# Kernel tuning notes

Measured on AMD Instinct MI355X. Metric: run time of the kernel, lower is better.

## Reference

```python
import jax, jax.numpy as jnp
import numpy as np

B, G, F = 256, 2048, 128   # batch, graph_size, feat_size (== gcn_dim == k)
RNN_DIM = 512
K = F  # self.k = args.gcn_dim


def setup_inputs() -> dict:
    key = jax.random.key(0)
    k1, k2, k3 = jax.random.split(key, 3)
    node_embs = jax.random.normal(k1, (B, G, F), dtype=jnp.float32)
    mask = jnp.zeros((B, G), dtype=jnp.float32)
    h_t = jax.random.normal(k2, (B, RNN_DIM), dtype=jnp.float32)
    W_map = jax.random.normal(k3, (RNN_DIM, F), dtype=jnp.float32) * (1.0 / np.sqrt(RNN_DIM))
    b_map = jnp.zeros((F,), dtype=jnp.float32)
    return {"node_embs": node_embs, "mask": mask, "h_t": h_t, "W_map": W_map, "b_map": b_map}


def reference(node_embs, mask, h_t, W_map, b_map):
    # mapper: Linear + Tanh -> scorer [B, F]
    scorer = jnp.tanh(h_t @ W_map + b_map)
    # scores = bmm(node_embs, scorer) / ||scorer||  -> [B, G]
    norm = jnp.linalg.norm(scorer, axis=1, keepdims=True)  # [B, 1]
    scores = jnp.einsum('bgf,bf->bg', node_embs, scorer) / norm
    scores = scores + mask
    # top-k over graph dim (mask is all-zero so no -inf filtering/padding needed)
    vals, topk_indices = jax.lax.top_k(scores, K)  # [B, K]
    # gather node embeddings at topk indices, scale by tanh of gathered scores
    gathered = jnp.take_along_axis(node_embs, topk_indices[:, :, None], axis=1)  # [B, K, F]
    out = gathered * jnp.tanh(vals)[:, :, None]  # tanh(scores.gather) == tanh(vals)
    # log-softmax over graph dim, gather at topk, mean -> policy score [B]
    log_probs = jax.nn.log_softmax(scores, axis=-1)
    score = jnp.take_along_axis(log_probs, topk_indices, axis=-1)  # [B, K]
    policy_score = score.mean(axis=1)
    return (jnp.transpose(out, (0, 2, 1)), policy_score)  # ([B, F, K], [B])
```

## Files before the change

kernel.cpp:

```cpp
#include <hip/hip_runtime.h>
#include <cmath>

#define B_ 256
#define G_ 2048
#define F_ 128
#define RNN_ 512
#define K_ 128

__global__ __launch_bounds__(1024) void k_fused(const float* __restrict__ node,
                                                const float* __restrict__ mask,
                                                const float* __restrict__ h_t,
                                                const float* __restrict__ W,
                                                const float* __restrict__ b_map,
                                                float* __restrict__ out,
                                                float* __restrict__ policy) {
    __shared__ __align__(16) float sc[G_];
    __shared__ unsigned hist[2][8][256];
    __shared__ __align__(16) float tile[K_][33];
    __shared__ __align__(16) float sn[F_];
    __shared__ unsigned long long win[K_];
    __shared__ float valk[K_];
    __shared__ float tanhv[K_];
    __shared__ int idxk[K_];
    __shared__ float red16[16];
    __shared__ unsigned long long prefix_sh;
    __shared__ int need_sh;
    __shared__ int done_sh;
    __shared__ int cnt;

    const int b = blockIdx.x;
    const int tid = threadIdx.x;
    const int wv = tid >> 6;
    const int lane = tid & 63;

    float* hsm = &tile[0][0];
    float(*wp)[F_] = (float(*)[F_])(hsm + RNN_);
    if (tid < RNN_) hsm[tid] = h_t[b * RNN_ + tid];
    if (tid == 0) { cnt = 0; done_sh = 0; }
    for (int i = tid; i < 8 * 256; i += 1024) ((unsigned*)hist[0])[i] = 0u;
    __syncthreads();
    {
        const int f = tid & 127;
        const int qu = tid >> 7;
        float acc = 0.f;
        const int r0 = qu * (RNN_ / 8);
#pragma unroll 8
        for (int r = r0; r < r0 + RNN_ / 8; ++r) acc += hsm[r] * W[r * F_ + f];
        wp[qu][f] = acc;
    }
    __syncthreads();
    float tval = 0.f;
    if (tid < F_) {
        float a = b_map[tid];
#pragma unroll
        for (int q = 0; q < 8; ++q) a += wp[q][tid];
        tval = tanhf(a);
    }
    float v = tval * tval;
#pragma unroll
    for (int off = 32; off; off >>= 1) v += __shfl_xor(v, off);
    if (tid == 0) red16[0] = v;
    if (tid == 64) red16[1] = v;
    __syncthreads();
    if (tid < F_) sn[tid] = tval / sqrtf(red16[0] + red16[1]);
    __syncthreads();

    {
        const int hw = tid >> 5;
        const int l32 = tid & 31;
        const float4 s4 = ((const float4*)sn)[l32];
        const float4* nb = (const float4*)(node + (size_t)b * (G_ * F_));
#pragma unroll 2
        for (int r = 0; r < 64; r += 4) {
            const float4 e0 = nb[(size_t)(((r + 0) << 5) + hw) * 32 + l32];
            const float4 e1 = nb[(size_t)(((r + 1) << 5) + hw) * 32 + l32];
            const float4 e2 = nb[(size_t)(((r + 2) << 5) + hw) * 32 + l32];
            const float4 e3 = nb[(size_t)(((r + 3) << 5) + hw) * 32 + l32];
            float p0 = e0.x * s4.x + e0.y * s4.y + e0.z * s4.z + e0.w * s4.w;
            float p1 = e1.x * s4.x + e1.y * s4.y + e1.z * s4.z + e1.w * s4.w;
            float p2 = e2.x * s4.x + e2.y * s4.y + e2.z * s4.z + e2.w * s4.w;
            float p3 = e3.x * s4.x + e3.y * s4.y + e3.z * s4.z + e3.w * s4.w;
#pragma unroll
            for (int off = 16; off; off >>= 1) {
                p0 += __shfl_xor(p0, off);
                p1 += __shfl_xor(p1, off);
                p2 += __shfl_xor(p2, off);
                p3 += __shfl_xor(p3, off);
            }
            if (l32 == 0) {
                sc[((r + 0) << 5) + hw] = p0;
                sc[((r + 1) << 5) + hw] = p1;
                sc[((r + 2) << 5) + hw] = p2;
                sc[((r + 3) << 5) + hw] = p3;
            }
        }
    }
    __syncthreads();

    unsigned long long kreg[2];
    float vv0, vv1;
    {
        const float2 v2 = ((const float2*)sc)[tid];
        const float2 m2 = ((const float2*)(mask + (size_t)b * G_))[tid];
        vv0 = v2.x + m2.x;
        vv1 = v2.y + m2.y;
        float2 wb;
        wb.x = vv0;
        wb.y = vv1;
        ((float2*)sc)[tid] = wb;
        unsigned u0 = __float_as_uint(vv0);
        u0 = (u0 & 0x80000000u) ? ~u0 : (u0 | 0x80000000u);
        kreg[0] = ((unsigned long long)u0 << 32) | (unsigned)(G_ - 1 - (2 * tid + 0));
        unsigned u1 = __float_as_uint(vv1);
        u1 = (u1 & 0x80000000u) ? ~u1 : (u1 | 0x80000000u);
        kreg[1] = ((unsigned long long)u1 << 32) | (unsigned)(G_ - 1 - (2 * tid + 1));
    }
    __syncthreads();

    unsigned long long prefix = 0ull;
    int need = K_;
    int round = 0;
    const int wv8 = wv & 7;
    for (int shift = 56; shift >= 0; shift -= 8, ++round) {
        unsigned(*H)[256] = hist[round & 1];
        const unsigned long long hi_mask = (shift == 56) ? 0ull : (~0ull << (shift + 8));
#pragma unroll
        for (int p = 0; p < 2; ++p) {
            const unsigned long long key = kreg[p];
            if ((key & hi_mask) == prefix)
                atomicAdd(&H[wv8][(unsigned)(key >> shift) & 255u], 1u);
        }
        __syncthreads();
        if (wv == 0) {
            const int L = lane;
            unsigned h0 = 0, h1 = 0, h2 = 0, h3 = 0;
#pragma unroll
            for (int ww = 0; ww < 8; ++ww) {
                h0 += H[ww][4 * L + 0];
                h1 += H[ww][4 * L + 1];
                h2 += H[ww][4 * L + 2];
                h3 += H[ww][4 * L + 3];
            }
            const unsigned s3 = h3, s2 = h2 + s3, s1 = h1 + s2, s0 = h0 + s1;
            unsigned S = s0;
            for (int off = 1; off < 64; off <<= 1) {
                const unsigned tt = __shfl_down(S, off);
                if (L + off < 64) S += tt;
            }
            unsigned Snext = __shfl_down(S, 1);
            if (L == 63) Snext = 0;
            const unsigned un = (unsigned)need;
            const unsigned suf0 = Snext + s0, suf1 = Snext + s1;
            const unsigned suf2 = Snext + s2, suf3 = Snext + s3, suf4 = Snext;
            int d = -1;
            unsigned sd = 0, sd1 = 0;
            if (suf0 >= un && suf1 < un) { d = 4 * L + 0; sd = suf0; sd1 = suf1; }
            else if (suf1 >= un && suf2 < un) { d = 4 * L + 1; sd = suf1; sd1 = suf2; }
            else if (suf2 >= un && suf3 < un) { d = 4 * L + 2; sd = suf2; sd1 = suf3; }
            else if (suf3 >= un && suf4 < un) { d = 4 * L + 3; sd = suf3; sd1 = suf4; }
            if (d >= 0) {
                prefix_sh = prefix | ((unsigned long long)(unsigned)d << shift);
                need_sh = need - (int)sd1;
                done_sh = (sd == un);
            }
        } else {
            unsigned* Z = (unsigned*)hist[(round + 1) & 1];
            for (int i = tid - 64; i < 8 * 256; i += 1024 - 64) Z[i] = 0u;
        }
        __syncthreads();
        prefix = prefix_sh;
        need = need_sh;
        if (done_sh) break;
    }
    const unsigned long long T = prefix;

#pragma unroll
    for (int p = 0; p < 2; ++p) {
        if (kreg[p] >= T) {
            const int q = atomicAdd(&cnt, 1);
            if (q < K_) win[q] = kreg[p];
        }
    }
    __syncthreads();
    if (tid < K_) {
        const unsigned long long mykey = win[tid];
        int rank = 0;
#pragma unroll 8
        for (int j = 0; j < K_; ++j) rank += (win[j] > mykey) ? 1 : 0;
        const int idx = G_ - 1 - (int)(unsigned)(mykey & 0xFFFFFFFFull);
        const float val = sc[idx];
        idxk[rank] = idx;
        valk[rank] = val;
        tanhv[rank] = tanhf(val);
    }
    __syncthreads();

    const float maxv = valk[0];
    float s = expf(vv0 - maxv) + expf(vv1 - maxv);
#pragma unroll
    for (int off = 32; off; off >>= 1) s += __shfl_xor(s, off);
    if (lane == 0) red16[wv] = s;
    __syncthreads();
    if (tid == 0) {
        float tot = 0.f;
#pragma unroll
        for (int i = 0; i < 16; ++i) tot += red16[i];
        const float lse = maxv + logf(tot);
        float sum = 0.f;
        for (int k = 0; k < K_; ++k) sum += valk[k];
        policy[b] = sum * (1.0f / K_) - lse;
    }

    const float* nbase = node + (size_t)b * (G_ * F_);
    float* ob = out + (size_t)b * (F_ * K_);
    const int k2 = tid >> 3;
    const int q8 = tid & 7;
    float4 pre = *(const float4*)(nbase + (size_t)idxk[k2] * F_ + 4 * q8);
    for (int f0 = 0; f0 < F_; f0 += 32) {
        tile[k2][4 * q8 + 0] = pre.x;
        tile[k2][4 * q8 + 1] = pre.y;
        tile[k2][4 * q8 + 2] = pre.z;
        tile[k2][4 * q8 + 3] = pre.w;
        __syncthreads();
        if (f0 + 32 < F_)
            pre = *(const float4*)(nbase + (size_t)idxk[k2] * F_ + (f0 + 32) + 4 * q8);
#pragma unroll
        for (int j = 0; j < 4; ++j) {
            const int e = tid + j * 1024;
            const int f = e >> 7;
            const int kk = e & 127;
            ob[(size_t)(f0 + f) * K_ + kk] = tile[kk][f] * tanhv[kk];
        }
        __syncthreads();
    }
}

extern "C" void kernel_launch(void* const* d_in, const int* in_sizes, int n_in,
                              void* d_out, int out_size, void* d_ws, size_t ws_size,
                              hipStream_t stream) {
    const float* node = (const float*)d_in[0];
    const float* mask = (const float*)d_in[1];
    const float* h_t = (const float*)d_in[2];
    const float* W = (const float*)d_in[3];
    const float* bm = (const float*)d_in[4];

    float* out = (float*)d_out;
    float* policy = out + (size_t)B_ * F_ * K_;

    k_fused<<<B_, 1024, 0, stream>>>(node, mask, h_t, W, bm, out, policy);
}
```

Measured before the change: 377.5 us.

## Overlay shared buffers, gather full rows at once, vectorize transposed output stores

Shared memory is unioned into one buffer reused across phases, so the gather stage can stage a full 128x129 tile instead of four 32-column passes with syncs. All four row-chunk gathers are issued before the log-sum-exp reduction to overlap their latency. The output is written with float4 stores, and the top-k value sum is done with a parallel shuffle reduction instead of a serial loop. The scoring loop is unrolled to 8 loads in flight, which raises register pressure.

```diff
diff --git a/kernel.cpp b/kernel.cpp
--- a/kernel.cpp
+++ b/kernel.cpp
@@ -14,27 +14,28 @@
                                                 const float* __restrict__ b_map,
                                                 float* __restrict__ out,
                                                 float* __restrict__ policy) {
-    __shared__ __align__(16) float sc[G_];
-    __shared__ unsigned hist[2][8][256];
-    __shared__ __align__(16) float tile[K_][33];
-    __shared__ __align__(16) float sn[F_];
+    __shared__ __align__(16) float u[128 * 129];
     __shared__ unsigned long long win[K_];
     __shared__ float valk[K_];
     __shared__ float tanhv[K_];
     __shared__ int idxk[K_];
     __shared__ float red16[16];
+    __shared__ float vsum2[2];
     __shared__ unsigned long long prefix_sh;
     __shared__ int need_sh;
     __shared__ int done_sh;
     __shared__ int cnt;
 
+    float* sc = u;
+    unsigned(*hist)[8][256] = (unsigned(*)[8][256])(u + 2048);
+    float* hsm = u + 2048 + 4096;
+    float(*wp)[F_] = (float(*)[F_])(hsm + RNN_);
+
     const int b = blockIdx.x;
     const int tid = threadIdx.x;
     const int wv = tid >> 6;
     const int lane = tid & 63;
 
-    float* hsm = &tile[0][0];
-    float(*wp)[F_] = (float(*)[F_])(hsm + RNN_);
     if (tid < RNN_) hsm[tid] = h_t[b * RNN_ + tid];
     if (tid == 0) { cnt = 0; done_sh = 0; }
     for (int i = tid; i < 8 * 256; i += 1024) ((unsigned*)hist[0])[i] = 0u;
@@ -62,36 +63,31 @@
     if (tid == 0) red16[0] = v;
     if (tid == 64) red16[1] = v;
     __syncthreads();
-    if (tid < F_) sn[tid] = tval / sqrtf(red16[0] + red16[1]);
+    if (tid < F_) hsm[tid] = tval / sqrtf(red16[0] + red16[1]);
     __syncthreads();
 
     {
         const int hw = tid >> 5;
         const int l32 = tid & 31;
-        const float4 s4 = ((const float4*)sn)[l32];
+        const float4 s4 = ((const float4*)hsm)[l32];
         const float4* nb = (const float4*)(node + (size_t)b * (G_ * F_));
-#pragma unroll 2
-        for (int r = 0; r < 64; r += 4) {
-            const float4 e0 = nb[(size_t)(((r + 0) << 5) + hw) * 32 + l32];
-            const float4 e1 = nb[(size_t)(((r + 1) << 5) + hw) * 32 + l32];
-            const float4 e2 = nb[(size_t)(((r + 2) << 5) + hw) * 32 + l32];
-            const float4 e3 = nb[(size_t)(((r + 3) << 5) + hw) * 32 + l32];
-            float p0 = e0.x * s4.x + e0.y * s4.y + e0.z * s4.z + e0.w * s4.w;
-            float p1 = e1.x * s4.x + e1.y * s4.y + e1.z * s4.z + e1.w * s4.w;
-            float p2 = e2.x * s4.x + e2.y * s4.y + e2.z * s4.z + e2.w * s4.w;
-            float p3 = e3.x * s4.x + e3.y * s4.y + e3.z * s4.z + e3.w * s4.w;
+        for (int r = 0; r < 64; r += 8) {
+            float4 e[8];
+#pragma unroll
+            for (int i = 0; i < 8; ++i)
+                e[i] = nb[(size_t)(((r + i) << 5) + hw) * 32 + l32];
+            float p[8];
+#pragma unroll
+            for (int i = 0; i < 8; ++i)
+                p[i] = e[i].x * s4.x + e[i].y * s4.y + e[i].z * s4.z + e[i].w * s4.w;
 #pragma unroll
             for (int off = 16; off; off >>= 1) {
-                p0 += __shfl_xor(p0, off);
-                p1 += __shfl_xor(p1, off);
-                p2 += __shfl_xor(p2, off);
-                p3 += __shfl_xor(p3, off);
+#pragma unroll
+                for (int i = 0; i < 8; ++i) p[i] += __shfl_xor(p[i], off);
             }
             if (l32 == 0) {
-                sc[((r + 0) << 5) + hw] = p0;
-                sc[((r + 1) << 5) + hw] = p1;
-                sc[((r + 2) << 5) + hw] = p2;
-                sc[((r + 3) << 5) + hw] = p3;
+#pragma unroll
+                for (int i = 0; i < 8; ++i) sc[((r + i) << 5) + hw] = p[i];
             }
         }
     }
@@ -196,42 +192,54 @@
     __syncthreads();
 
     const float maxv = valk[0];
-    float s = expf(vv0 - maxv) + expf(vv1 - maxv);
-#pragma unroll
-    for (int off = 32; off; off >>= 1) s += __shfl_xor(s, off);
-    if (lane == 0) red16[wv] = s;
-    __syncthreads();
-    if (tid == 0) {
-        float tot = 0.f;
-#pragma unroll
-        for (int i = 0; i < 16; ++i) tot += red16[i];
-        const float lse = maxv + logf(tot);
-        float sum = 0.f;
-        for (int k = 0; k < K_; ++k) sum += valk[k];
-        policy[b] = sum * (1.0f / K_) - lse;
-    }
-
     const float* nbase = node + (size_t)b * (G_ * F_);
     float* ob = out + (size_t)b * (F_ * K_);
     const int k2 = tid >> 3;
     const int q8 = tid & 7;
-    float4 pre = *(const float4*)(nbase + (size_t)idxk[k2] * F_ + 4 * q8);
-    for (int f0 = 0; f0 < F_; f0 += 32) {
-        tile[k2][4 * q8 + 0] = pre.x;
-        tile[k2][4 * q8 + 1] = pre.y;
-        tile[k2][4 * q8 + 2] = pre.z;
-        tile[k2][4 * q8 + 3] = pre.w;
-        __syncthreads();
-        if (f0 + 32 < F_)
-            pre = *(const float4*)(nbase + (size_t)idxk[k2] * F_ + (f0 + 32) + 4 * q8);
-#pragma unroll
-        for (int j = 0; j < 4; ++j) {
-            const int e = tid + j * 1024;
-            const int f = e >> 7;
-            const int kk = e & 127;
-            ob[(size_t)(f0 + f) * K_ + kk] = tile[kk][f] * tanhv[kk];
-        }
-        __syncthreads();
+    const float* nrow = nbase + (size_t)idxk[k2] * F_ + 4 * q8;
+    const float4 g0 = *(const float4*)(nrow + 0);
+    const float4 g1 = *(const float4*)(nrow + 32);
+    const float4 g2 = *(const float4*)(nrow + 64);
+    const float4 g3 = *(const float4*)(nrow + 96);
+
+    float s = expf(vv0 - maxv) + expf(vv1 - maxv);
+#pragma unroll
+    for (int off = 32; off; off >>= 1) s += __shfl_xor(s, off);
+    if (lane == 0) red16[wv] = s;
+    if (tid < 128) {
+        float pv = valk[tid];
+#pragma unroll
+        for (int off = 32; off; off >>= 1) pv += __shfl_xor(pv, off);
+        if ((tid & 63) == 0) vsum2[tid >> 6] = pv;
+    }
+    __syncthreads();
+    if (tid == 0) {
+        float tot = 0.f;
+#pragma unroll
+        for (int i = 0; i < 16; ++i) tot += red16[i];
+        policy[b] = (vsum2[0] + vsum2[1]) * (1.0f / K_) - (maxv + logf(tot));
+    }
+
+    float(*tE)[129] = (float(*)[129])u;
+    {
+        float* tr = &tE[k2][4 * q8];
+        tr[0] = g0.x;  tr[1] = g0.y;  tr[2] = g0.z;  tr[3] = g0.w;
+        tr[32] = g1.x; tr[33] = g1.y; tr[34] = g1.z; tr[35] = g1.w;
+        tr[64] = g2.x; tr[65] = g2.y; tr[66] = g2.z; tr[67] = g2.w;
+        tr[96] = g3.x; tr[97] = g3.y; tr[98] = g3.z; tr[99] = g3.w;
+    }
+    __syncthreads();
+#pragma unroll
+    for (int j = 0; j < 4; ++j) {
+        const int e4 = tid + j * 1024;
+        const int f = e4 >> 5;
+        const int k4 = (e4 & 31) << 2;
+        float4 o;
+        o.x = tE[k4 + 0][f] * tanhv[k4 + 0];
+        o.y = tE[k4 + 1][f] * tanhv[k4 + 1];
+        o.z = tE[k4 + 2][f] * tanhv[k4 + 2];
+        o.w = tE[k4 + 3][f] * tanhv[k4 + 3];
+        *(float4*)(ob + (size_t)f * K_ + k4) = o;
     }
 }
 
```

New measurement: 378.9 us. About the same (+0.4%).
